# Optimization experiments

Measured on AMD Instinct MI355X. Metric: run time of the kernel, lower is better.

The kernel has to match this reference:

```python
import jax, jax.numpy as jnp
import numpy as np

B, T, S, D, H, DK, DV, DFF = 2, 2048, 2048, 1024, 16, 64, 64, 4096
EPS = 1e-5


def layer_norm(x, g, b):
    m = jnp.mean(x, axis=-1, keepdims=True)
    v = jnp.var(x, axis=-1, keepdims=True)
    return (x - m) * jax.lax.rsqrt(v + EPS) * g + b


def mha(q_in, k_in, v_in, Wq, bq, Wk, bk, Wv, bv, Wo, bo, mask):
    # q_in: [B, Lq, D]; k_in/v_in: [B, Lk, D]
    Q = (q_in @ Wq + bq).reshape(q_in.shape[0], -1, H, DK).transpose(0, 2, 1, 3)  # [B,H,Lq,dk]
    K = (k_in @ Wk + bk).reshape(k_in.shape[0], -1, H, DK).transpose(0, 2, 1, 3)
    V = (v_in @ Wv + bv).reshape(v_in.shape[0], -1, H, DV).transpose(0, 2, 1, 3)
    scores = jnp.einsum('bhqd,bhkd->bhqk', Q, K) / jnp.float32(np.sqrt(DK))
    scores = jnp.where(mask == 0, jnp.float32(-1e9), scores)
    attn = jax.nn.softmax(scores, axis=-1)
    out = jnp.einsum('bhqk,bhkd->bhqd', attn, V)
    out = out.transpose(0, 2, 1, 3).reshape(q_in.shape[0], -1, H * DV)
    return out @ Wo + bo


def setup_inputs() -> dict:
    key = jax.random.key(0)
    ks = jax.random.split(key, 16)
    s = 0.02
    inp = {
        'x': jax.random.normal(ks[0], (B, T, D), jnp.float32),
        'encoder_output': jax.random.normal(ks[1], (B, S, D), jnp.float32),
        'lookahead_mask': jnp.tril(jnp.ones((T, T), jnp.int32))[None, None],  # [1,1,T,T]
        'padding_mask': jnp.ones((1, 1, 1, S), jnp.int32),
        # self-attention params
        'sa_Wq': jax.random.normal(ks[2], (D, H * DK), jnp.float32) * s,
        'sa_bq': jnp.zeros((H * DK,), jnp.float32),
        'sa_Wk': jax.random.normal(ks[3], (D, H * DK), jnp.float32) * s,
        'sa_bk': jnp.zeros((H * DK,), jnp.float32),
        'sa_Wv': jax.random.normal(ks[4], (D, H * DV), jnp.float32) * s,
        'sa_bv': jnp.zeros((H * DV,), jnp.float32),
        'sa_Wo': jax.random.normal(ks[5], (H * DV, D), jnp.float32) * s,
        'sa_bo': jnp.zeros((D,), jnp.float32),
        # cross-attention params
        'ca_Wq': jax.random.normal(ks[6], (D, H * DK), jnp.float32) * s,
        'ca_bq': jnp.zeros((H * DK,), jnp.float32),
        'ca_Wk': jax.random.normal(ks[7], (D, H * DK), jnp.float32) * s,
        'ca_bk': jnp.zeros((H * DK,), jnp.float32),
        'ca_Wv': jax.random.normal(ks[8], (D, H * DV), jnp.float32) * s,
        'ca_bv': jnp.zeros((H * DV,), jnp.float32),
        'ca_Wo': jax.random.normal(ks[9], (H * DV, D), jnp.float32) * s,
        'ca_bo': jnp.zeros((D,), jnp.float32),
        # feed-forward params
        'ff_W1': jax.random.normal(ks[10], (D, DFF), jnp.float32) * s,
        'ff_b1': jnp.zeros((DFF,), jnp.float32),
        'ff_W2': jax.random.normal(ks[11], (DFF, D), jnp.float32) * s,
        'ff_b2': jnp.zeros((D,), jnp.float32),
        # layer norms
        'ln1_g': jnp.ones((D,), jnp.float32), 'ln1_b': jnp.zeros((D,), jnp.float32),
        'ln2_g': jnp.ones((D,), jnp.float32), 'ln2_b': jnp.zeros((D,), jnp.float32),
        'ln3_g': jnp.ones((D,), jnp.float32), 'ln3_b': jnp.zeros((D,), jnp.float32),
    }
    return inp


def reference(x, encoder_output, lookahead_mask, padding_mask,
              sa_Wq, sa_bq, sa_Wk, sa_bk, sa_Wv, sa_bv, sa_Wo, sa_bo,
              ca_Wq, ca_bq, ca_Wk, ca_bk, ca_Wv, ca_bv, ca_Wo, ca_bo,
              ff_W1, ff_b1, ff_W2, ff_b2,
              ln1_g, ln1_b, ln2_g, ln2_b, ln3_g, ln3_b):
    attn1 = mha(x, x, x, sa_Wq, sa_bq, sa_Wk, sa_bk, sa_Wv, sa_bv, sa_Wo, sa_bo, lookahead_mask)
    addnorm1 = layer_norm(x + attn1, ln1_g, ln1_b)
    attn2 = mha(addnorm1, encoder_output, encoder_output,
                ca_Wq, ca_bq, ca_Wk, ca_bk, ca_Wv, ca_bv, ca_Wo, ca_bo, padding_mask)
    addnorm2 = layer_norm(addnorm1 + attn2, ln2_g, ln2_b)
    ff = jax.nn.relu(addnorm2 @ ff_W1 + ff_b1) @ ff_W2 + ff_b2
    return layer_norm(addnorm2 + ff, ln3_g, ln3_b)
```

## Files before the change

### kernel.cpp

```cpp
#include <hip/hip_runtime.h>

typedef unsigned short u16;
typedef unsigned int   u32;
typedef __attribute__((ext_vector_type(8)))  __bf16 bf16x8;
typedef __attribute__((ext_vector_type(4)))  float  f32x4;
typedef __attribute__((ext_vector_type(16))) float  f32x16;
typedef __attribute__((ext_vector_type(4)))  unsigned short u16x4;

#define DEV static __device__ __forceinline__

#define SC 0.1803368801111243f

DEV u16 cvt_bf16(float f){
  u32 u = __builtin_bit_cast(u32, f);
  u32 r = (u + 0x7FFFu + ((u >> 16) & 1u)) >> 16;
  return (u16)r;
}

typedef __attribute__((address_space(1))) void* as1p;
typedef __attribute__((address_space(3))) void* as3p;

DEV void gld16(void* lds, const void* g){
  __builtin_amdgcn_global_load_lds((as1p)g, (as3p)lds, 16, 0, 0);
}

DEV f32x4 mfma16(bf16x8 a, bf16x8 b, f32x4 c){
  return __builtin_amdgcn_mfma_f32_16x16x32_bf16(a, b, c, 0, 0, 0);
}
DEV f32x16 mfma32(bf16x8 a, bf16x8 b, f32x16 c){
  return __builtin_amdgcn_mfma_f32_32x32x16_bf16(a, b, c, 0, 0, 0);
}

DEV bf16x8 ld8(const u16* p){ return *(const bf16x8*)p; }

DEV float vexp2(float x){
  float y; asm("v_exp_f32 %0, %1" : "=v"(y) : "v"(x)); return y;
}

DEV u32 cvtpk(float lo, float hi){
  u32 r; asm("v_cvt_pk_bf16_f32 %0, %1, %2" : "=v"(r) : "v"(lo), "v"(hi)); return r;
}
DEV void perm32swap(u32 &a, u32 &b){
  asm("v_permlane32_swap_b32 %0, %1" : "+v"(a), "+v"(b));
}
DEV bf16x8 frag4(u32 w0,u32 w1,u32 w2,u32 w3){
  union{ u32 w[4]; bf16x8 f; } u; u.w[0]=w0; u.w[1]=w1; u.w[2]=w2; u.w[3]=w3; return u.f;
}

DEV int swz64(int row, int blk){ return row*64 + ((blk ^ (row & 7)) << 3); }
DEV int swz32(int row, int blk){ return row*32 + ((blk ^ (row & 3)) << 3); }

__global__ __launch_bounds__(256) void castk2(const float* __restrict__ in0,
                                              u16* __restrict__ out0,
                                              const float* __restrict__ in1,
                                              u16* __restrict__ out1){
  const float* in = blockIdx.y ? in1 : in0;
  u16*        out = blockIdx.y ? out1 : out0;
  int i = blockIdx.x*256 + threadIdx.x;
  f32x4 v = *(const f32x4*)(in + (size_t)i*4);
  u16x4 o;
  #pragma unroll
  for(int j=0;j<4;j++) o[j] = cvt_bf16(v[j]);
  *(u16x4*)(out + (size_t)i*4) = o;
}

__global__ __launch_bounds__(256) void smallfuse(
    const float* __restrict__ sabq, const float* __restrict__ sabk,
    const float* __restrict__ sabv, const float* __restrict__ cabk,
    const float* __restrict__ cabv, const int* __restrict__ pm,
    float* __restrict__ bqkv, float* __restrict__ bkvc, float* __restrict__ biasg){
  int i = blockIdx.x*256 + threadIdx.x;
  if(i < 1024)       bqkv[i] = sabq[i];
  else if(i < 2048)  bqkv[i] = sabk[i-1024];
  else if(i < 3072)  bqkv[i] = sabv[i-2048];
  else if(i < 4096)  bkvc[i-3072] = cabk[i-3072];
  else if(i < 5120)  bkvc[i-3072] = cabv[i-4096];
  else if(i < 7168)  biasg[i-5120] = pm[i-5120] ? 0.f : -8e9f;
}

DEV void wcast_body(const float* __restrict__ W, u16* __restrict__ Wt,
                    int K, int N, int bx, int by, int tid){
  __shared__ u16 tile[64][66];
  const int k0 = bx*64, n0 = by*64;
  const int lr = tid >> 4, c4 = (tid & 15)*4;
  #pragma unroll
  for(int p=0;p<4;p++){
    const int r = lr + p*16;
    f32x4 v = *(const f32x4*)&W[(size_t)(k0+r)*N + n0 + c4];
    #pragma unroll
    for(int j=0;j<4;j++) tile[r][c4+j] = cvt_bf16(v[j]);
  }
  __syncthreads();
  #pragma unroll
  for(int p=0;p<4;p++){
    const int n = lr + p*16;
    u16x4 u;
    #pragma unroll
    for(int j=0;j<4;j++) u[j] = tile[c4+j][n];
    *(u16x4*)&Wt[(size_t)(n0+n)*K + k0 + c4] = u;
  }
}

__global__ __launch_bounds__(256) void wcast_t(const float* __restrict__ W,
                                               u16* __restrict__ Wt, int K, int N){
  wcast_body(W, Wt, K, N, blockIdx.x, blockIdx.y, threadIdx.x);
}

__global__ __launch_bounds__(256) void wcast8(
    const float* s0, const float* s1, const float* s2, const float* s3,
    const float* s4, const float* s5, const float* s6, const float* s7,
    u16* d0, u16* d1, u16* d2, u16* d3, u16* d4, u16* d5, u16* d6, u16* d7){
  const float* W; u16* Wt;
  switch(blockIdx.z){
    case 0: W=s0; Wt=d0; break;  case 1: W=s1; Wt=d1; break;
    case 2: W=s2; Wt=d2; break;  case 3: W=s3; Wt=d3; break;
    case 4: W=s4; Wt=d4; break;  case 5: W=s5; Wt=d5; break;
    case 6: W=s6; Wt=d6; break;  default: W=s7; Wt=d7; break;
  }
  wcast_body(W, Wt, 1024, 1024, blockIdx.x, blockIdx.y, threadIdx.x);
}

__global__ __launch_bounds__(256) void vtrans(const u16* __restrict__ V,
                                              u16* __restrict__ Vt, int L, int ld){
  __shared__ u16 tile[64][66];
  const int t0 = blockIdx.x*64;
  const int h = blockIdx.y, b = blockIdx.z;
  const int lr = threadIdx.x >> 4, c4 = (threadIdx.x & 15)*4;
  #pragma unroll
  for(int p=0;p<4;p++){
    const int r = lr + p*16;
    u16x4 v = *(const u16x4*)&V[(size_t)(b*L + t0 + r)*ld + h*64 + c4];
    #pragma unroll
    for(int j=0;j<4;j++) tile[r][c4+j] = v[j];
  }
  __syncthreads();
  #pragma unroll
  for(int p=0;p<4;p++){
    const int d = lr + p*16;
    u16x4 u;
    #pragma unroll
    for(int j=0;j<4;j++) u[j] = tile[c4+j][d];
    *(u16x4*)&Vt[((size_t)((b*16 + h)*64 + d))*L + t0 + c4] = u;
  }
}

template<int OMODE, int BN, int SPLITK>
__global__ __launch_bounds__(256, BN==128 ? 3 : 4) void gemm_bt(
    const u16* __restrict__ A, const u16* __restrict__ Bt,
    const float* __restrict__ bias, void* __restrict__ Cout0, void* __restrict__ Cout1,
    int N, int K)
{
  __shared__ __align__(16) u16 As[2][128*32];
  __shared__ __align__(16) u16 Bs[2][BN*32];
  constexpr int NJ = BN/32;
  const int tid = threadIdx.x, wave = tid>>6, lane = tid&63;
  const int fr = lane&15, fg = lane>>4;
  const int bm = blockIdx.x*128, bn = blockIdx.y*BN;
  const int part = (SPLITK>1) ? blockIdx.z : 0;
  const int Kp = K / SPLITK;
  const int kbase = part * Kp;
  const int wm = (wave>>1)*64, wn = (wave&1)*(BN/2);
  const f32x4 z4 = {0.f,0.f,0.f,0.f};
  f32x4 acc[4][NJ];
  #pragma unroll
  for(int i=0;i<4;i++)
    #pragma unroll
    for(int j=0;j<NJ;j++) acc[i][j] = z4;

  const int srA = wave*32 + (lane>>2);
  const int cl_l = (lane&3)*8;
  const int cl_g = ((lane&3) ^ ((lane>>2)&3))*8;
  const int srB = (BN==128) ? srA : (wave*16 + (lane>>2));
  const u16* gA = A  + (size_t)(bm + srA)*K + kbase + cl_g;
  const u16* gB = Bt + (size_t)(bn + srB)*K + kbase + cl_g;

  auto stage = [&](int p, int ko){
    u16* lA = &As[p][srA*32 + cl_l];
    u16* lB = &Bs[p][srB*32 + cl_l];
    gld16(lA,     gA + ko);
    gld16(lA+512, gA + ko + (size_t)16*K);
    gld16(lB,     gB + ko);
    if(BN==128) gld16(lB+512, gB + ko + (size_t)16*K);
  };

  const int nk = Kp >> 5;
  stage(0, 0);
  __syncthreads();
  for(int kt=0; kt<nk; ++kt){
    const int cur = kt & 1;
    if(kt+1 < nk) stage(cur^1, (kt+1)*32);
    bf16x8 af[4], bfv[NJ];
    #pragma unroll
    for(int i=0;i<4;i++) af[i] = ld8(&As[cur][swz32(wm + i*16 + fr, fg)]);
    #pragma unroll
    for(int j=0;j<NJ;j++) bfv[j] = ld8(&Bs[cur][swz32(wn + j*16 + fr, fg)]);
    __builtin_amdgcn_s_setprio(1);
    #pragma unroll
    for(int i=0;i<4;i++)
      #pragma unroll
      for(int j=0;j<NJ;j++)
        acc[i][j] = mfma16(af[i], bfv[j], acc[i][j]);
    __builtin_amdgcn_s_setprio(0);
    __syncthreads();
  }

  void* Cout = (part==0) ? Cout0 : Cout1;
  const int r0 = bm + wm + fg*4;
  const int c0 = bn + wn + fr;
  #pragma unroll
  for(int j=0;j<NJ;j++){
    const int col = c0 + j*16;
    const float bv = (part==0) ? bias[col] : 0.f;
    #pragma unroll
    for(int i=0;i<4;i++){
      #pragma unroll
      for(int r=0;r<4;r++){
        const float v = acc[i][j][r] + bv;
        const size_t idx = (size_t)(r0 + i*16 + r)*N + col;
        if(OMODE==0)      ((float*)Cout)[idx] = v;
        else if(OMODE==1) ((u16*)Cout)[idx]   = cvt_bf16(v);
        else              ((u16*)Cout)[idx]   = cvt_bf16(fmaxf(v, 0.f));
      }
    }
  }
}

template<bool CAUSAL>
__global__ __launch_bounds__(256,4) void attn3(
    const u16* __restrict__ Qg, int ldq, const u16* __restrict__ Kg, int ldk,
    const u16* __restrict__ Vt, const float* __restrict__ biasg,
    float* __restrict__ Opart, float* __restrict__ Ml, float* __restrict__ Ll,
    int Lk)
{
  __shared__ __align__(16) u16 Ks[2][64*64];
  __shared__ __align__(16) u16 Vs[2][64*64];
  __shared__ float FacL[4][32];
  const int tid = threadIdx.x, wave = tid>>6, lane = tid&63;
  const int l31 = lane&31, hi = lane>>5;
  const int bid = blockIdx.x;
  const int g    = (bid&7)*4 + (bid>>8);
  const int r5   = (bid>>3)&31;
  const int part = r5&1, qb = r5>>1;
  const int h = g&15, b = g>>4;
  const int qi = CAUSAL ? ((qb&1) ? (15-(qb>>1)) : (qb>>1)) : qb;
  const int q0 = qi*128;
  const int qw = q0 + wave*32;
  const int qrow = qw + l31;

  bf16x8 qf[4];
  {
    const u16* Qp = Qg + (size_t)(b*2048 + qrow)*ldq + h*64;
    #pragma unroll
    for(int c=0;c<4;c++) qf[c] = ld8(Qp + c*16 + hi*8);
  }

  f32x16 o0, o1;
  #pragma unroll
  for(int r=0;r<16;r++){ o0[r]=0.f; o1[r]=0.f; }
  float m = -3e38f, lsum = 0.f;

  const int srow = wave*16 + (lane>>3);
  const int cl_l = (lane&7)*8;
  const int cl_g = ((lane&7) ^ ((lane>>3)&7))*8;
  const u16* Kp = Kg + (size_t)(b*2048 + srow)*ldk + h*64 + cl_g;
  const u16* Vp = Vt + ((size_t)((b*16 + h)*64 + srow))*Lk + cl_g;

  auto stage = [&](int p, int kv0){
    u16* lK = &Ks[p][srow*64 + cl_l];
    u16* lV = &Vs[p][srow*64 + cl_l];
    gld16(lK,     Kp + (size_t)kv0*ldk);
    gld16(lK+512, Kp + (size_t)(kv0+8)*ldk);
    gld16(lV,     Vp + kv0);
    gld16(lV+512, Vp + kv0 + 8*(size_t)Lk);
  };

  const int span = CAUSAL ? (qi+1) : ((Lk>>6)>>1);
  const int t0 = part*span, t1 = t0 + span;

  stage(0, t0*64);
  __syncthreads();
  for(int kt=t0; kt<t1; ++kt){
    const int cur = (kt-t0)&1;
    const int kv0 = kt*64;
    if(kt+1 < t1) stage(cur^1, (kt+1)*64);

    if(!CAUSAL || kv0 <= qw+31){
      f32x16 s0, s1;
      #pragma unroll
      for(int r=0;r<16;r++){ s0[r]=0.f; s1[r]=0.f; }
      __builtin_amdgcn_s_setprio(1);
      #pragma unroll
      for(int c=0;c<4;c++){
        bf16x8 k0 = ld8(&Ks[cur][swz64(l31,      2*c+hi)]);
        bf16x8 k1 = ld8(&Ks[cur][swz64(32 + l31, 2*c+hi)]);
        s0 = mfma32(k0, qf[c], s0);
        s1 = mfma32(k1, qf[c], s1);
      }
      __builtin_amdgcn_s_setprio(0);

      float p[32];
      #pragma unroll
      for(int r=0;r<16;r++){ p[r]=s0[r]; p[16+r]=s1[r]; }

      if(CAUSAL){
        if(kv0 + 63 > qw){
          #pragma unroll
          for(int n=0;n<2;n++)
            #pragma unroll
            for(int r=0;r<16;r++){
              const int kc = kv0 + 32*n + (r&3) + 8*(r>>2) + 4*hi;
              if(kc > qrow) p[16*n+r] = -8e9f;
            }
        }
      } else {
        #pragma unroll
        for(int n=0;n<2;n++)
          #pragma unroll
          for(int cq=0;cq<4;cq++){
            f32x4 bv = *(const f32x4*)&biasg[kv0 + 32*n + 8*cq + 4*hi];
            #pragma unroll
            for(int i=0;i<4;i++) p[16*n+4*cq+i] += bv[i];
          }
      }

      float pm = p[0];
      #pragma unroll
      for(int r=1;r<32;r++) pm = fmaxf(pm, p[r]);
      pm = fmaxf(pm, __shfl_xor(pm, 32));
      if(__any(pm > m + 64.f)){
        const float nm = fmaxf(m, pm);
        const float fac = vexp2((m - nm)*SC);
        lsum *= fac;
        FacL[wave][l31] = fac;
        #pragma unroll
        for(int r=0;r<16;r++){
          const int qidx = (r&3) + 8*(r>>2) + 4*hi;
          const float fb = FacL[wave][qidx];
          o0[r] *= fb; o1[r] *= fb;
        }
        m = nm;
      }
      float rs = 0.f;
      #pragma unroll
      for(int r=0;r<32;r++){ p[r] = vexp2((p[r]-m)*SC); rs += p[r]; }
      rs += __shfl_xor(rs, 32);
      lsum += rs;

      u32 pw[16];
      #pragma unroll
      for(int n=0;n<2;n++)
        #pragma unroll
        for(int cp=0;cp<2;cp++){
          const int base = 16*n + 8*cp, cc = 2*n + cp;
          u32 a1 = cvtpk(p[base+0], p[base+1]);
          u32 a2 = cvtpk(p[base+2], p[base+3]);
          u32 b1 = cvtpk(p[base+4], p[base+5]);
          u32 b2 = cvtpk(p[base+6], p[base+7]);
          perm32swap(a1, b1);
          perm32swap(a2, b2);
          pw[4*cc+0]=a1; pw[4*cc+1]=a2; pw[4*cc+2]=b1; pw[4*cc+3]=b2;
        }

      __builtin_amdgcn_s_setprio(1);
      #pragma unroll
      for(int cc=0;cc<4;cc++){
        bf16x8 pf = frag4(pw[4*cc], pw[4*cc+1], pw[4*cc+2], pw[4*cc+3]);
        bf16x8 v0 = ld8(&Vs[cur][swz64(l31,      2*cc+hi)]);
        bf16x8 v1 = ld8(&Vs[cur][swz64(32 + l31, 2*cc+hi)]);
        o0 = mfma32(pf, v0, o0);
        o1 = mfma32(pf, v1, o1);
      }
      __builtin_amdgcn_s_setprio(0);
    }
    __syncthreads();
  }

  float* Op = Opart + (size_t)part*4194304 + (size_t)(b*2048 + qw)*1024 + h*64;
  #pragma unroll
  for(int r=0;r<16;r++){
    const int qidx = (r&3) + 8*(r>>2) + 4*hi;
    Op[(size_t)qidx*1024 + l31]      = o0[r];
    Op[(size_t)qidx*1024 + 32 + l31] = o1[r];
  }
  if(hi==0){
    const int mi = part*65536 + (b*2048 + qw + l31)*16 + h;
    Ml[mi] = m; Ll[mi] = lsum;
  }
}

__global__ __launch_bounds__(256) void att_combine(
    const float* __restrict__ O0, const float* __restrict__ O1,
    const float* __restrict__ Ml, const float* __restrict__ Ll,
    u16* __restrict__ Ob)
{
  const int row = blockIdx.x, tid = threadIdx.x;
  const int h = tid>>4;
  const int mi = row*16 + h;
  const float m0 = Ml[mi], m1 = Ml[65536+mi];
  const float l0 = Ll[mi], l1 = Ll[65536+mi];
  const float mx = fmaxf(m0, m1);
  const float w0 = vexp2((m0-mx)*SC), w1 = vexp2((m1-mx)*SC);
  const float inv = 1.f/(w0*l0 + w1*l1);
  const size_t base = (size_t)row*1024 + tid*4;
  f32x4 a = *(const f32x4*)(O0 + base);
  f32x4 c = *(const f32x4*)(O1 + base);
  u16x4 o;
  #pragma unroll
  for(int j=0;j<4;j++) o[j] = cvt_bf16((w0*a[j] + w1*c[j])*inv);
  *(u16x4*)(Ob + base) = o;
}

__global__ __launch_bounds__(256) void add_ln3(const float* __restrict__ X,
                        const float* __restrict__ D1, const float* __restrict__ D2,
                        const float* __restrict__ gam, const float* __restrict__ bet,
                        float* __restrict__ outf, u16* __restrict__ outb){
  __shared__ float red[8];
  const int tid = threadIdx.x, wave = tid>>6, lane = tid&63;
  const size_t base = ((size_t)blockIdx.x << 10) + tid*4;
  f32x4 xv = *(const f32x4*)(X + base);
  f32x4 d1 = *(const f32x4*)(D1 + base);
  f32x4 d2 = *(const f32x4*)(D2 + base);
  f32x4 v;
  #pragma unroll
  for(int j=0;j<4;j++) v[j] = xv[j] + d1[j] + d2[j];
  float s = v[0]+v[1]+v[2]+v[3];
  float q = v[0]*v[0]+v[1]*v[1]+v[2]*v[2]+v[3]*v[3];
  #pragma unroll
  for(int off=1;off<64;off<<=1){ s += __shfl_xor(s,off); q += __shfl_xor(q,off); }
  if(lane==0){ red[wave]=s; red[4+wave]=q; }
  __syncthreads();
  s = red[0]+red[1]+red[2]+red[3];
  q = red[4]+red[5]+red[6]+red[7];
  const float mean = s*(1.f/1024.f);
  const float var  = q*(1.f/1024.f) - mean*mean;
  const float rr = rsqrtf(var + 1e-5f);
  const int c = tid*4;
  f32x4 y;
  #pragma unroll
  for(int j=0;j<4;j++) y[j] = (v[j]-mean)*rr*gam[c+j] + bet[c+j];
  *(f32x4*)(outf + base) = y;
  if(outb){
    u16x4 ob;
    #pragma unroll
    for(int j=0;j<4;j++) ob[j] = cvt_bf16(y[j]);
    *(u16x4*)(outb + base) = ob;
  }
}

extern "C" void kernel_launch(void* const* d_in, const int* in_sizes, int n_in,
                              void* d_out, int out_size, void* d_ws, size_t ws_size,
                              hipStream_t stream)
{
  (void)in_sizes; (void)n_in; (void)out_size; (void)ws_size;
  const float* x    = (const float*)d_in[0];
  const float* enc  = (const float*)d_in[1];
  const int*   pmask= (const int*)d_in[3];
  const float* saWq = (const float*)d_in[4];  const float* sabq = (const float*)d_in[5];
  const float* saWk = (const float*)d_in[6];  const float* sabk = (const float*)d_in[7];
  const float* saWv = (const float*)d_in[8];  const float* sabv = (const float*)d_in[9];
  const float* saWo = (const float*)d_in[10]; const float* sabo = (const float*)d_in[11];
  const float* caWq = (const float*)d_in[12]; const float* cabq = (const float*)d_in[13];
  const float* caWk = (const float*)d_in[14]; const float* cabk = (const float*)d_in[15];
  const float* caWv = (const float*)d_in[16]; const float* cabv = (const float*)d_in[17];
  const float* caWo = (const float*)d_in[18]; const float* cabo = (const float*)d_in[19];
  const float* fW1  = (const float*)d_in[20]; const float* fb1  = (const float*)d_in[21];
  const float* fW2  = (const float*)d_in[22]; const float* fb2  = (const float*)d_in[23];
  const float* l1g  = (const float*)d_in[24]; const float* l1b  = (const float*)d_in[25];
  const float* l2g  = (const float*)d_in[26]; const float* l2b  = (const float*)d_in[27];
  const float* l3g  = (const float*)d_in[28]; const float* l3b  = (const float*)d_in[29];

  char* wsp = (char*)d_ws;
  size_t off = 0;
  auto take = [&](size_t bytes)->void*{ void* p = wsp + off; off += (bytes + 255) & ~(size_t)255; return p; };
  u16* slotA  = (u16*)take(8388608);
  u16* Encb   = (u16*)take(8388608);
  u16* WqkvT  = (u16*)take(6291456);
  u16* cWqT   = (u16*)take(2097152);
  u16* cWkvT  = (u16*)take(4194304);
  u16* WoT    = (u16*)take(2097152);
  u16* cWoT   = (u16*)take(2097152);
  u16* W1T    = (u16*)take(8388608);
  u16* W2T    = (u16*)take(8388608);
  float* bqkv = (float*)take(16384);
  float* bkvc = (float*)take(16384);
  float* biasg= (float*)take(16384);
  u16* slotB  = (u16*)take(25165824);
  u16* Vtb    = (u16*)take(8388608);
  u16* Ob     = (u16*)take(8388608);
  u16* an1b   = (u16*)take(8388608);
  float* projf= (float*)take(16777216);
  float* an1f = (float*)take(16777216);
  float* an2f = (float*)take(16777216);
  char* ffhb  = (char*)take(33554432);
  u16* Xbf = slotA;  u16* Qcb = slotA;  u16* an2b = slotA;
  u16* QKVb = slotB; u16* KVc = slotB;
  u16* ffh   = (u16*)ffhb;
  float* Opar = (float*)ffhb;
  float* Mlb = (float*)an1b;
  float* Llb = Mlb + 131072;

  castk2<<<dim3(4096,2),256,0,stream>>>(x, Xbf, enc, Encb);
  wcast8<<<dim3(16,16,8),256,0,stream>>>(
      saWq, saWk, saWv, saWo, caWq, caWk, caWv, caWo,
      WqkvT, WqkvT + 1024*1024, WqkvT + 2*1024*1024, WoT,
      cWqT, cWkvT, cWkvT + 1024*1024, cWoT);
  wcast_t<<<dim3(16,64),256,0,stream>>>(fW1, W1T, 1024, 4096);
  wcast_t<<<dim3(64,16),256,0,stream>>>(fW2, W2T, 4096, 1024);
  smallfuse<<<28,256,0,stream>>>(sabq, sabk, sabv, cabk, cabv, pmask,
                                 bqkv, bkvc, biasg);

  gemm_bt<1,128,1><<<dim3(32,24),256,0,stream>>>(Xbf, WqkvT, bqkv, QKVb, nullptr, 3072, 1024);
  vtrans<<<dim3(32,16,2),256,0,stream>>>(QKVb + 2048, Vtb, 2048, 3072);
  attn3<true><<<1024,256,0,stream>>>(QKVb, 3072, QKVb + 1024, 3072, Vtb, nullptr,
                                     Opar, Mlb, Llb, 2048);
  att_combine<<<4096,256,0,stream>>>(Opar, Opar + 4194304, Mlb, Llb, Ob);
  gemm_bt<0,128,2><<<dim3(32,8,2),256,0,stream>>>(Ob, WoT, sabo, projf, an2f, 1024, 1024);
  add_ln3<<<4096,256,0,stream>>>(x, projf, an2f, l1g, l1b, an1f, an1b);

  gemm_bt<1,64,1><<<dim3(32,16),256,0,stream>>>(an1b, cWqT, cabq, Qcb, nullptr, 1024, 1024);
  gemm_bt<1,128,1><<<dim3(32,16),256,0,stream>>>(Encb, cWkvT, bkvc, KVc, nullptr, 2048, 1024);
  vtrans<<<dim3(32,16,2),256,0,stream>>>(KVc + 1024, Vtb, 2048, 2048);
  attn3<false><<<1024,256,0,stream>>>(Qcb, 1024, KVc, 2048, Vtb, biasg,
                                      Opar, Mlb, Llb, 2048);
  att_combine<<<4096,256,0,stream>>>(Opar, Opar + 4194304, Mlb, Llb, Ob);
  gemm_bt<0,128,2><<<dim3(32,8,2),256,0,stream>>>(Ob, cWoT, cabo, projf, Opar, 1024, 1024);
  add_ln3<<<4096,256,0,stream>>>(an1f, projf, Opar, l2g, l2b, an2f, an2b);

  gemm_bt<2,128,1><<<dim3(32,32),256,0,stream>>>(an2b, W1T, fb1, ffh, nullptr, 4096, 1024);
  gemm_bt<0,128,2><<<dim3(32,8,2),256,0,stream>>>(ffh, W2T, fb2, projf, an1f, 1024, 4096);
  add_ln3<<<4096,256,0,stream>>>(an2f, projf, an1f, l3g, l3b, (float*)d_out, nullptr);
}
```

Measured before the change: 422.8 us.

## Fold softmax scale into Q weights and split causal attention four ways

Pre-multiplies the Q projection weights and biases by the log2e/sqrt(dk) factor during the bf16 cast, so the attention inner loop can call exp2 directly without a per-element multiply. Causal self-attention now splits its KV range into four parts (2048 blocks) instead of two. The combine kernel is generalised to N partitions. The LDS rescale table is replaced with a lane shuffle, the rescale threshold is tightened, and occupancy bounds are raised to 5. The risks are extra partial-output traffic and register pressure from the higher occupancy target.

```diff
diff --git a/kernel.cpp b/kernel.cpp
--- a/kernel.cpp
+++ b/kernel.cpp
@@ -67,19 +67,22 @@
 __global__ __launch_bounds__(256) void smallfuse(
     const float* __restrict__ sabq, const float* __restrict__ sabk,
     const float* __restrict__ sabv, const float* __restrict__ cabk,
-    const float* __restrict__ cabv, const int* __restrict__ pm,
-    float* __restrict__ bqkv, float* __restrict__ bkvc, float* __restrict__ biasg){
+    const float* __restrict__ cabv, const float* __restrict__ cabq,
+    const int* __restrict__ pm,
+    float* __restrict__ bqkv, float* __restrict__ bkvc,
+    float* __restrict__ biasg, float* __restrict__ bqc){
   int i = blockIdx.x*256 + threadIdx.x;
-  if(i < 1024)       bqkv[i] = sabq[i];
+  if(i < 1024)       bqkv[i] = sabq[i]*SC;
   else if(i < 2048)  bqkv[i] = sabk[i-1024];
   else if(i < 3072)  bqkv[i] = sabv[i-2048];
   else if(i < 4096)  bkvc[i-3072] = cabk[i-3072];
   else if(i < 5120)  bkvc[i-3072] = cabv[i-4096];
-  else if(i < 7168)  biasg[i-5120] = pm[i-5120] ? 0.f : -8e9f;
+  else if(i < 7168)  biasg[i-5120] = pm[i-5120] ? 0.f : -1e9f;
+  else if(i < 8192)  bqc[i-7168] = cabq[i-7168]*SC;
 }
 
 DEV void wcast_body(const float* __restrict__ W, u16* __restrict__ Wt,
-                    int K, int N, int bx, int by, int tid){
+                    int K, int N, int bx, int by, int tid, float scale){
   __shared__ u16 tile[64][66];
   const int k0 = bx*64, n0 = by*64;
   const int lr = tid >> 4, c4 = (tid & 15)*4;
@@ -88,7 +91,7 @@
     const int r = lr + p*16;
     f32x4 v = *(const f32x4*)&W[(size_t)(k0+r)*N + n0 + c4];
     #pragma unroll
-    for(int j=0;j<4;j++) tile[r][c4+j] = cvt_bf16(v[j]);
+    for(int j=0;j<4;j++) tile[r][c4+j] = cvt_bf16(v[j]*scale);
   }
   __syncthreads();
   #pragma unroll
@@ -103,7 +106,7 @@
 
 __global__ __launch_bounds__(256) void wcast_t(const float* __restrict__ W,
                                                u16* __restrict__ Wt, int K, int N){
-  wcast_body(W, Wt, K, N, blockIdx.x, blockIdx.y, threadIdx.x);
+  wcast_body(W, Wt, K, N, blockIdx.x, blockIdx.y, threadIdx.x, 1.f);
 }
 
 __global__ __launch_bounds__(256) void wcast8(
@@ -117,7 +120,8 @@
     case 4: W=s4; Wt=d4; break;  case 5: W=s5; Wt=d5; break;
     case 6: W=s6; Wt=d6; break;  default: W=s7; Wt=d7; break;
   }
-  wcast_body(W, Wt, 1024, 1024, blockIdx.x, blockIdx.y, threadIdx.x);
+  const float scale = (blockIdx.z==0 || blockIdx.z==4) ? SC : 1.f;
+  wcast_body(W, Wt, 1024, 1024, blockIdx.x, blockIdx.y, threadIdx.x, scale);
 }
 
 __global__ __launch_bounds__(256) void vtrans(const u16* __restrict__ V,
@@ -225,8 +229,8 @@
   }
 }
 
-template<bool CAUSAL>
-__global__ __launch_bounds__(256,4) void attn3(
+template<bool CAUSAL, int NPART>
+__global__ __launch_bounds__(256,5) void attn3(
     const u16* __restrict__ Qg, int ldq, const u16* __restrict__ Kg, int ldk,
     const u16* __restrict__ Vt, const float* __restrict__ biasg,
     float* __restrict__ Opart, float* __restrict__ Ml, float* __restrict__ Ll,
@@ -234,13 +238,13 @@
 {
   __shared__ __align__(16) u16 Ks[2][64*64];
   __shared__ __align__(16) u16 Vs[2][64*64];
-  __shared__ float FacL[4][32];
+  constexpr int P2 = NPART*16;
   const int tid = threadIdx.x, wave = tid>>6, lane = tid&63;
   const int l31 = lane&31, hi = lane>>5;
   const int bid = blockIdx.x;
-  const int g    = (bid&7)*4 + (bid>>8);
-  const int r5   = (bid>>3)&31;
-  const int part = r5&1, qb = r5>>1;
+  const int g    = (bid&7)*4 + ((bid>>3)/P2);
+  const int rp   = (bid>>3)%P2;
+  const int part = rp&(NPART-1), qb = rp/NPART;
   const int h = g&15, b = g>>4;
   const int qi = CAUSAL ? ((qb&1) ? (15-(qb>>1)) : (qb>>1)) : qb;
   const int q0 = qi*128;
@@ -274,8 +278,8 @@
     gld16(lV+512, Vp + kv0 + 8*(size_t)Lk);
   };
 
-  const int span = CAUSAL ? (qi+1) : ((Lk>>6)>>1);
-  const int t0 = part*span, t1 = t0 + span;
+  const int T  = CAUSAL ? (2*qi+2) : (Lk>>6);
+  const int t0 = part*T/NPART, t1 = (part+1)*T/NPART;
 
   stage(0, t0*64);
   __syncthreads();
@@ -309,7 +313,7 @@
             #pragma unroll
             for(int r=0;r<16;r++){
               const int kc = kv0 + 32*n + (r&3) + 8*(r>>2) + 4*hi;
-              if(kc > qrow) p[16*n+r] = -8e9f;
+              if(kc > qrow) p[16*n+r] = -1e9f;
             }
         }
       } else {
@@ -323,26 +327,25 @@
           }
       }
 
-      float pm = p[0];
-      #pragma unroll
-      for(int r=1;r<32;r++) pm = fmaxf(pm, p[r]);
+      float pm = fmaxf(p[30], p[31]);
+      #pragma unroll
+      for(int r=0;r<30;r+=2) pm = fmaxf(pm, fmaxf(p[r], p[r+1]));
       pm = fmaxf(pm, __shfl_xor(pm, 32));
-      if(__any(pm > m + 64.f)){
+      if(__any(pm > m + 8.f)){
         const float nm = fmaxf(m, pm);
-        const float fac = vexp2((m - nm)*SC);
+        const float fac = vexp2(m - nm);
         lsum *= fac;
-        FacL[wave][l31] = fac;
         #pragma unroll
         for(int r=0;r<16;r++){
           const int qidx = (r&3) + 8*(r>>2) + 4*hi;
-          const float fb = FacL[wave][qidx];
+          const float fb = __shfl(fac, qidx);
           o0[r] *= fb; o1[r] *= fb;
         }
         m = nm;
       }
       float rs = 0.f;
       #pragma unroll
-      for(int r=0;r<32;r++){ p[r] = vexp2((p[r]-m)*SC); rs += p[r]; }
+      for(int r=0;r<32;r++){ p[r] = vexp2(p[r]-m); rs += p[r]; }
       rs += __shfl_xor(rs, 32);
       lsum += rs;
 
@@ -388,25 +391,37 @@
   }
 }
 
+template<int NP>
 __global__ __launch_bounds__(256) void att_combine(
-    const float* __restrict__ O0, const float* __restrict__ O1,
-    const float* __restrict__ Ml, const float* __restrict__ Ll,
-    u16* __restrict__ Ob)
+    const float* __restrict__ O, const float* __restrict__ Ml,
+    const float* __restrict__ Ll, u16* __restrict__ Ob)
 {
   const int row = blockIdx.x, tid = threadIdx.x;
   const int h = tid>>4;
   const int mi = row*16 + h;
-  const float m0 = Ml[mi], m1 = Ml[65536+mi];
-  const float l0 = Ll[mi], l1 = Ll[65536+mi];
-  const float mx = fmaxf(m0, m1);
-  const float w0 = vexp2((m0-mx)*SC), w1 = vexp2((m1-mx)*SC);
-  const float inv = 1.f/(w0*l0 + w1*l1);
+  float mv[NP], lv[NP];
+  float mx = -3e38f;
+  #pragma unroll
+  for(int p=0;p<NP;p++){
+    mv[p] = Ml[p*65536 + mi];
+    lv[p] = Ll[p*65536 + mi];
+    mx = fmaxf(mx, mv[p]);
+  }
+  float w[NP], denom = 0.f;
+  #pragma unroll
+  for(int p=0;p<NP;p++){ w[p] = vexp2(mv[p]-mx); denom += w[p]*lv[p]; }
+  const float inv = 1.f/denom;
   const size_t base = (size_t)row*1024 + tid*4;
-  f32x4 a = *(const f32x4*)(O0 + base);
-  f32x4 c = *(const f32x4*)(O1 + base);
+  f32x4 acc = {0.f,0.f,0.f,0.f};
+  #pragma unroll
+  for(int p=0;p<NP;p++){
+    f32x4 a = *(const f32x4*)(O + (size_t)p*4194304 + base);
+    #pragma unroll
+    for(int j=0;j<4;j++) acc[j] += w[p]*a[j];
+  }
   u16x4 o;
   #pragma unroll
-  for(int j=0;j<4;j++) o[j] = cvt_bf16((w0*a[j] + w1*c[j])*inv);
+  for(int j=0;j<4;j++) o[j] = cvt_bf16(acc[j]*inv);
   *(u16x4*)(Ob + base) = o;
 }
 
@@ -484,6 +499,7 @@
   float* bqkv = (float*)take(16384);
   float* bkvc = (float*)take(16384);
   float* biasg= (float*)take(16384);
+  float* bqc  = (float*)take(16384);
   u16* slotB  = (u16*)take(25165824);
   u16* Vtb    = (u16*)take(8388608);
   u16* Ob     = (u16*)take(8388608);
@@ -495,9 +511,10 @@
   u16* Xbf = slotA;  u16* Qcb = slotA;  u16* an2b = slotA;
   u16* QKVb = slotB; u16* KVc = slotB;
   u16* ffh   = (u16*)ffhb;
-  float* Opar = (float*)ffhb;
+  float* OparS = projf;
+  float* OparC = (float*)ffhb;
   float* Mlb = (float*)an1b;
-  float* Llb = Mlb + 131072;
+  float* Llb = Mlb + 4*65536;
 
   castk2<<<dim3(4096,2),256,0,stream>>>(x, Xbf, enc, Encb);
   wcast8<<<dim3(16,16,8),256,0,stream>>>(
@@ -506,25 +523,25 @@
       cWqT, cWkvT, cWkvT + 1024*1024, cWoT);
   wcast_t<<<dim3(16,64),256,0,stream>>>(fW1, W1T, 1024, 4096);
   wcast_t<<<dim3(64,16),256,0,stream>>>(fW2, W2T, 4096, 1024);
-  smallfuse<<<28,256,0,stream>>>(sabq, sabk, sabv, cabk, cabv, pmask,
-                                 bqkv, bkvc, biasg);
+  smallfuse<<<32,256,0,stream>>>(sabq, sabk, sabv, cabk, cabv, cabq, pmask,
+                                 bqkv, bkvc, biasg, bqc);
 
   gemm_bt<1,128,1><<<dim3(32,24),256,0,stream>>>(Xbf, WqkvT, bqkv, QKVb, nullptr, 3072, 1024);
   vtrans<<<dim3(32,16,2),256,0,stream>>>(QKVb + 2048, Vtb, 2048, 3072);
-  attn3<true><<<1024,256,0,stream>>>(QKVb, 3072, QKVb + 1024, 3072, Vtb, nullptr,
-                                     Opar, Mlb, Llb, 2048);
-  att_combine<<<4096,256,0,stream>>>(Opar, Opar + 4194304, Mlb, Llb, Ob);
+  attn3<true,4><<<2048,256,0,stream>>>(QKVb, 3072, QKVb + 1024, 3072, Vtb, nullptr,
+                                       OparS, Mlb, Llb, 2048);
+  att_combine<4><<<4096,256,0,stream>>>(OparS, Mlb, Llb, Ob);
   gemm_bt<0,128,2><<<dim3(32,8,2),256,0,stream>>>(Ob, WoT, sabo, projf, an2f, 1024, 1024);
   add_ln3<<<4096,256,0,stream>>>(x, projf, an2f, l1g, l1b, an1f, an1b);
 
-  gemm_bt<1,64,1><<<dim3(32,16),256,0,stream>>>(an1b, cWqT, cabq, Qcb, nullptr, 1024, 1024);
+  gemm_bt<1,64,1><<<dim3(32,16),256,0,stream>>>(an1b, cWqT, bqc, Qcb, nullptr, 1024, 1024);
   gemm_bt<1,128,1><<<dim3(32,16),256,0,stream>>>(Encb, cWkvT, bkvc, KVc, nullptr, 2048, 1024);
   vtrans<<<dim3(32,16,2),256,0,stream>>>(KVc + 1024, Vtb, 2048, 2048);
-  attn3<false><<<1024,256,0,stream>>>(Qcb, 1024, KVc, 2048, Vtb, biasg,
-                                      Opar, Mlb, Llb, 2048);
-  att_combine<<<4096,256,0,stream>>>(Opar, Opar + 4194304, Mlb, Llb, Ob);
-  gemm_bt<0,128,2><<<dim3(32,8,2),256,0,stream>>>(Ob, cWoT, cabo, projf, Opar, 1024, 1024);
-  add_ln3<<<4096,256,0,stream>>>(an1f, projf, Opar, l2g, l2b, an2f, an2b);
+  attn3<false,2><<<1024,256,0,stream>>>(Qcb, 1024, KVc, 2048, Vtb, biasg,
+                                        OparC, Mlb, Llb, 2048);
+  att_combine<2><<<4096,256,0,stream>>>(OparC, Mlb, Llb, Ob);
+  gemm_bt<0,128,2><<<dim3(32,8,2),256,0,stream>>>(Ob, cWoT, cabo, projf, OparC, 1024, 1024);
+  add_ln3<<<4096,256,0,stream>>>(an1f, projf, OparC, l2g, l2b, an2f, an2b);
 
   gemm_bt<2,128,1><<<dim3(32,32),256,0,stream>>>(an2b, W1T, fb1, ffh, nullptr, 4096, 1024);
   gemm_bt<0,128,2><<<dim3(32,8,2),256,0,stream>>>(ffh, W2T, fb2, projf, an1f, 1024, 4096);
```

New measurement: 500.6 us. +18.4%, slower.
